# Optimization experiments

Hardware: AMD Instinct MI355X
Metric: run time of the kernel (lower is better)

Reference implementation:

```python
import jax, jax.numpy as jnp
import numpy as np

B, T, F, U = 64, 1024, 128, 256


def setup_inputs() -> dict:
    key = jax.random.key(0)
    k1, k2, k3 = jax.random.split(key, 3)
    inputs = jax.random.normal(k1, (B, T, F), dtype=jnp.float32)
    # R ~ Normal(stddev=1/time_horizon)
    R = jax.random.normal(k2, (F, U), dtype=jnp.float32) / T
    # W ~ Orthogonal init
    a = jax.random.normal(k3, (U, U), dtype=jnp.float32)
    q, r = jnp.linalg.qr(a)
    W = q * jnp.sign(jnp.diag(r))[None, :]
    bias = jnp.zeros((U,), dtype=jnp.float32)
    x0 = jnp.zeros((U,), dtype=jnp.float32)
    return {"inputs": inputs, "R": R, "W": W, "bias": bias, "x0": x0}


def reference(inputs, R, W, bias, x0):
    # inputs: [B, T, F]. Precompute input projections for all steps at once.
    h_all = jnp.einsum("btf,fu->tbu", inputs, R)  # [T, B, U]
    state0 = jnp.broadcast_to(x0, (inputs.shape[0], x0.shape[0]))  # [B, U]

    def step(state, h):
        new_state = jnp.tanh(h + state @ W + bias)
        return new_state, new_state

    _, states = jax.lax.scan(step, state0, h_all)  # states: [T, B, U]
    return states
```

## Files before the change

kernel.cpp:

```cpp
#include <hip/hip_runtime.h>
#include <hip/hip_bf16.h>

constexpr int B = 64;
constexpr int T = 1024;
constexpr int F = 128;
constexpr int U = 256;
constexpr int CH = 8;

__device__ __forceinline__ float toF32(float v) { return v; }
__device__ __forceinline__ float toF32(__hip_bfloat16 v) { return __bfloat162float(v); }

__device__ __forceinline__ void store8(float* p, const float* a) {
    ((float4*)p)[0] = make_float4(a[0], a[1], a[2], a[3]);
    ((float4*)p)[1] = make_float4(a[4], a[5], a[6], a[7]);
}
__device__ __forceinline__ void store8(__hip_bfloat16* p, const float* a) {
    unsigned int v[4];
    #pragma unroll
    for (int i = 0; i < 4; ++i) {
        __hip_bfloat16 lo = __float2bfloat16(a[2 * i]);
        __hip_bfloat16 hi = __float2bfloat16(a[2 * i + 1]);
        unsigned short lob = *(unsigned short*)&lo;
        unsigned short hib = *(unsigned short*)&hi;
        v[i] = (unsigned int)lob | ((unsigned int)hib << 16);
    }
    ((uint4*)p)[0] = make_uint4(v[0], v[1], v[2], v[3]);
}

__device__ __forceinline__ float rdlane(float v, int l) {
    return __uint_as_float(__builtin_amdgcn_readlane(__float_as_uint(v), l));
}

__device__ __forceinline__ float tanh_fast(float x) {
    float e = __builtin_amdgcn_exp2f(x * 2.885390081777927f);
    float r = __builtin_amdgcn_rcpf(1.0f + e);
    return fmaf(-2.0f, r, 1.0f);
}

__device__ __forceinline__ void lds_barrier() {
    __builtin_amdgcn_s_waitcnt(0xC07F);
    asm volatile("" ::: "memory");
    __builtin_amdgcn_s_barrier();
    asm volatile("" ::: "memory");
}

template <typename HT>
__global__ __launch_bounds__(512, 2) void proj_kernel(
    const float* __restrict__ in,
    const float* __restrict__ Rm,
    HT* __restrict__ h)
{
    const int t0   = blockIdx.x * 64;
    const int u0b  = blockIdx.y * 64;
    const int b    = blockIdx.z;
    const int tid  = threadIdx.x;
    const int lane = tid & 63;
    const int wv   = tid >> 6;
    const int u0   = __builtin_amdgcn_readfirstlane(u0b + wv * 8);

    __shared__ float4 a4[64 * 32];

    const float4* src = (const float4*)(in + ((size_t)b * T + t0) * F);
    #pragma unroll
    for (int it = 0; it < 4; ++it) {
        int f  = tid + it * 512;
        int r  = f >> 5;
        int k4 = f & 31;
        a4[(r << 5) | (k4 ^ (r & 31))] = src[f];
    }
    __syncthreads();

    const float* Rp = Rm + u0;
    float acc[8];
    #pragma unroll
    for (int j = 0; j < 8; ++j) acc[j] = 0.f;

    float ra[32], rb[32];
    #pragma unroll
    for (int kk = 0; kk < 4; ++kk)
        #pragma unroll
        for (int j = 0; j < 8; ++j)
            ra[kk * 8 + j] = Rp[(size_t)kk * U + j];

    const int r = lane;
    #pragma unroll
    for (int k4 = 0; k4 < 32; k4 += 2) {
        #pragma unroll
        for (int kk = 0; kk < 4; ++kk)
            #pragma unroll
            for (int j = 0; j < 8; ++j)
                rb[kk * 8 + j] = Rp[(size_t)((k4 + 1) * 4 + kk) * U + j];

        float4 av = a4[(r << 5) | (k4 ^ (r & 31))];
        #pragma unroll
        for (int j = 0; j < 8; ++j) {
            acc[j] = fmaf(av.x, ra[0 * 8 + j], acc[j]);
            acc[j] = fmaf(av.y, ra[1 * 8 + j], acc[j]);
            acc[j] = fmaf(av.z, ra[2 * 8 + j], acc[j]);
            acc[j] = fmaf(av.w, ra[3 * 8 + j], acc[j]);
        }

        if (k4 + 2 < 32) {
            #pragma unroll
            for (int kk = 0; kk < 4; ++kk)
                #pragma unroll
                for (int j = 0; j < 8; ++j)
                    ra[kk * 8 + j] = Rp[(size_t)((k4 + 2) * 4 + kk) * U + j];
        }

        float4 av2 = a4[(r << 5) | ((k4 + 1) ^ (r & 31))];
        #pragma unroll
        for (int j = 0; j < 8; ++j) {
            acc[j] = fmaf(av2.x, rb[0 * 8 + j], acc[j]);
            acc[j] = fmaf(av2.y, rb[1 * 8 + j], acc[j]);
            acc[j] = fmaf(av2.z, rb[2 * 8 + j], acc[j]);
            acc[j] = fmaf(av2.w, rb[3 * 8 + j], acc[j]);
        }
    }

    HT* hp = h + ((size_t)(t0 + r) * B + b) * U + u0;
    store8(hp, acc);
}

template <typename HT>
__global__ __launch_bounds__(512, 2) void rnn_kernel(
    const HT* __restrict__ h,
    const float* __restrict__ Wm,
    const float* __restrict__ bias,
    const float* __restrict__ x0,
    float* __restrict__ out)
{
    const int b    = blockIdx.x;
    const int tid  = threadIdx.x;
    const int l    = tid & 63;
    const int wv   = tid >> 6;
    const int k0   = wv << 5;

    __shared__ float p[2][8][256];

    float w0[32], w1[32], w2[32], w3[32];
    {
        const float* wp = Wm + (size_t)k0 * U + 4 * l;
        #pragma unroll
        for (int kk = 0; kk < 32; ++kk) {
            float4 v = *(const float4*)(wp + (size_t)kk * U);
            w0[kk] = v.x; w1[kk] = v.y; w2[kk] = v.z; w3[kk] = v.w;
        }
    }

    const bool act = (l < 32);
    const int  u   = k0 + (l & 31);
    const float bv = bias[u];

    float tv = x0[u];

    const size_t sT = (size_t)B * U;
    const HT* hp = h + (size_t)b * U + u;
    float* op = out + (size_t)b * U + u;

    float hc[CH], hn[CH], ob[CH];
    #pragma unroll
    for (int i = 0; i < CH; ++i) hc[i] = toF32(hp[(size_t)i * sT]);

    for (int tc = 0; tc < T; tc += CH) {
        if (tc + CH < T) {
            #pragma unroll
            for (int i = 0; i < CH; ++i)
                hn[i] = toF32(hp[(size_t)(tc + CH + i) * sT]);
        }
        if (tc > 0 && act) {
            #pragma unroll
            for (int i = 0; i < CH; ++i)
                op[(size_t)(tc - CH + i) * sT] = ob[i];
        }

        #pragma unroll
        for (int i = 0; i < CH; ++i) {
            float sb[32];
            #pragma unroll
            for (int kk = 0; kk < 32; ++kk) sb[kk] = rdlane(tv, kk);

            float a0 = 0.f, a1 = 0.f, a2 = 0.f, a3 = 0.f;
            #pragma unroll
            for (int kk = 0; kk < 32; ++kk) {
                a0 = fmaf(sb[kk], w0[kk], a0);
                a1 = fmaf(sb[kk], w1[kk], a1);
                a2 = fmaf(sb[kk], w2[kk], a2);
                a3 = fmaf(sb[kk], w3[kk], a3);
            }
            *(float4*)&p[i & 1][wv][4 * l] = make_float4(a0, a1, a2, a3);

            lds_barrier();

            float red = p[i & 1][0][u];
            #pragma unroll
            for (int w2i = 1; w2i < 8; ++w2i) red += p[i & 1][w2i][u];

            float val = tanh_fast(red + hc[i] + bv);
            ob[i] = val;
            tv = val;
        }

        if (tc + CH < T) {
            #pragma unroll
            for (int i = 0; i < CH; ++i) hc[i] = hn[i];
        }
    }

    if (act) {
        #pragma unroll
        for (int i = 0; i < CH; ++i)
            op[(size_t)(T - CH + i) * sT] = ob[i];
    }
}

extern "C" void kernel_launch(void* const* d_in, const int* in_sizes, int n_in,
                              void* d_out, int out_size, void* d_ws, size_t ws_size,
                              hipStream_t stream) {
    const float* in   = (const float*)d_in[0];
    const float* Rm   = (const float*)d_in[1];
    const float* Wm   = (const float*)d_in[2];
    const float* bias = (const float*)d_in[3];
    const float* x0   = (const float*)d_in[4];
    float* out = (float*)d_out;

    const size_t hElems = (size_t)T * B * U;
    dim3 pgrid(T / 64, U / 64, B);

    if (ws_size >= hElems * sizeof(float)) {
        float* h = (float*)d_ws;
        proj_kernel<float><<<pgrid, 512, 0, stream>>>(in, Rm, h);
        rnn_kernel<float><<<dim3(B), 512, 0, stream>>>(h, Wm, bias, x0, out);
    } else {
        __hip_bfloat16* h = (__hip_bfloat16*)d_ws;
        proj_kernel<__hip_bfloat16><<<pgrid, 512, 0, stream>>>(in, Rm, h);
        rnn_kernel<__hip_bfloat16><<<dim3(B), 512, 0, stream>>>(h, Wm, bias, x0, out);
    }
}
```

Baseline: 670.0 us.

## Use packed fp16 dot2 for recurrent matvec with DPP pair packing

Converts the W slice held in registers to packed fp16 pairs and computes the state-times-W product with v_dot2_f32_f16. The neighbouring lane's state comes in through a DPP swap, and each readlane broadcasts two fp16 values at once. This halves both readlanes and FMAs on the serial critical path and cuts weight register use. The change also folds the bias into the preloaded h values and reduces the cross-wave partials as a balanced tree. In exchange, state and weights are rounded to fp16 every step, which can accumulate error over the 1024-step recurrence.

```diff
diff --git a/kernel.cpp b/kernel.cpp
--- a/kernel.cpp
+++ b/kernel.cpp
@@ -6,6 +6,8 @@
 constexpr int F = 128;
 constexpr int U = 256;
 constexpr int CH = 8;
+
+typedef __fp16 h2 __attribute__((ext_vector_type(2)));
 
 __device__ __forceinline__ float toF32(float v) { return v; }
 __device__ __forceinline__ float toF32(__hip_bfloat16 v) { return __bfloat162float(v); }
@@ -27,8 +29,24 @@
     ((uint4*)p)[0] = make_uint4(v[0], v[1], v[2], v[3]);
 }
 
-__device__ __forceinline__ float rdlane(float v, int l) {
-    return __uint_as_float(__builtin_amdgcn_readlane(__float_as_uint(v), l));
+__device__ __forceinline__ unsigned int h2bits(h2 v) {
+    union { h2 h; unsigned int u; } c; c.h = v; return c.u;
+}
+__device__ __forceinline__ h2 bits2h(unsigned int u) {
+    union { unsigned int u; h2 h; } c; c.u = u; return c.h;
+}
+
+__device__ __forceinline__ h2 pk_rne(float a, float b) {
+    h2 v; v.x = (__fp16)a; v.y = (__fp16)b; return v;
+}
+
+__device__ __forceinline__ float fdot2(h2 a, h2 b, float c) {
+#if __has_builtin(__builtin_amdgcn_fdot2)
+    return __builtin_amdgcn_fdot2(a, b, c, false);
+#else
+    asm("v_dot2_f32_f16 %0, %1, %2, %0" : "+v"(c) : "v"(a), "v"(b));
+    return c;
+#endif
 }
 
 __device__ __forceinline__ float tanh_fast(float x) {
@@ -138,13 +156,17 @@
 
     __shared__ float p[2][8][256];
 
-    float w0[32], w1[32], w2[32], w3[32];
+    h2 wh[4][16];
     {
         const float* wp = Wm + (size_t)k0 * U + 4 * l;
         #pragma unroll
-        for (int kk = 0; kk < 32; ++kk) {
-            float4 v = *(const float4*)(wp + (size_t)kk * U);
-            w0[kk] = v.x; w1[kk] = v.y; w2[kk] = v.z; w3[kk] = v.w;
+        for (int m = 0; m < 16; ++m) {
+            float4 r0 = *(const float4*)(wp + (size_t)(2 * m) * U);
+            float4 r1 = *(const float4*)(wp + (size_t)(2 * m + 1) * U);
+            wh[0][m] = pk_rne(r0.x, r1.x);
+            wh[1][m] = pk_rne(r0.y, r1.y);
+            wh[2][m] = pk_rne(r0.z, r1.z);
+            wh[3][m] = pk_rne(r0.w, r1.w);
         }
     }
 
@@ -160,7 +182,7 @@
 
     float hc[CH], hn[CH], ob[CH];
     #pragma unroll
-    for (int i = 0; i < CH; ++i) hc[i] = toF32(hp[(size_t)i * sT]);
+    for (int i = 0; i < CH; ++i) hc[i] = toF32(hp[(size_t)i * sT]) + bv;
 
     for (int tc = 0; tc < T; tc += CH) {
         if (tc + CH < T) {
@@ -176,34 +198,39 @@
 
         #pragma unroll
         for (int i = 0; i < CH; ++i) {
-            float sb[32];
-            #pragma unroll
-            for (int kk = 0; kk < 32; ++kk) sb[kk] = rdlane(tv, kk);
+            float nb = __uint_as_float(__builtin_amdgcn_update_dpp(
+                0, (int)__float_as_uint(tv), 0xB1 ,
+                0xF, 0xF, true));
+            unsigned int pku = h2bits(pk_rne(tv, nb));
 
             float a0 = 0.f, a1 = 0.f, a2 = 0.f, a3 = 0.f;
             #pragma unroll
-            for (int kk = 0; kk < 32; ++kk) {
-                a0 = fmaf(sb[kk], w0[kk], a0);
-                a1 = fmaf(sb[kk], w1[kk], a1);
-                a2 = fmaf(sb[kk], w2[kk], a2);
-                a3 = fmaf(sb[kk], w3[kk], a3);
+            for (int m = 0; m < 16; ++m) {
+                h2 sh = bits2h(__builtin_amdgcn_readlane(pku, 2 * m));
+                a0 = fdot2(sh, wh[0][m], a0);
+                a1 = fdot2(sh, wh[1][m], a1);
+                a2 = fdot2(sh, wh[2][m], a2);
+                a3 = fdot2(sh, wh[3][m], a3);
             }
             *(float4*)&p[i & 1][wv][4 * l] = make_float4(a0, a1, a2, a3);
 
             lds_barrier();
 
-            float red = p[i & 1][0][u];
-            #pragma unroll
-            for (int w2i = 1; w2i < 8; ++w2i) red += p[i & 1][w2i][u];
-
-            float val = tanh_fast(red + hc[i] + bv);
+            const float* pb = &p[i & 1][0][u];
+            float q0 = pb[0 * 256], q1 = pb[1 * 256];
+            float q2 = pb[2 * 256], q3 = pb[3 * 256];
+            float q4 = pb[4 * 256], q5 = pb[5 * 256];
+            float q6 = pb[6 * 256], q7 = pb[7 * 256];
+            float red = ((q0 + q1) + (q2 + q3)) + ((q4 + q5) + (q6 + q7));
+
+            float val = tanh_fast(red + hc[i]);
             ob[i] = val;
             tv = val;
         }
 
         if (tc + CH < T) {
             #pragma unroll
-            for (int i = 0; i < CH; ++i) hc[i] = hn[i];
+            for (int i = 0; i < CH; ++i) hc[i] = hn[i] + bv;
         }
     }
 
```

After: 722.5 us. 1.08x slower.

## Batch 8 sequences per block and compute recurrence matmul with fp16 MFMA

Applied to the files above, without the earlier changes.

The recurrent kernel now processes 8 batch rows per workgroup and computes state@W with 16x16x32 fp16 MFMA instructions, with W held in registers as fp16 fragments. The state is exchanged through a swizzled double-buffered fp16 LDS tile with one barrier per step. This replaces the per-lane readlane broadcast, scalar FMAs and cross-wave LDS reduction, cutting per-step latency. The launch drops to 8 blocks, and using fp16 for the state and weights may introduce accuracy error across the long recurrence.

```diff
diff --git a/kernel.cpp b/kernel.cpp
--- a/kernel.cpp
+++ b/kernel.cpp
@@ -5,7 +5,9 @@
 constexpr int T = 1024;
 constexpr int F = 128;
 constexpr int U = 256;
-constexpr int CH = 8;
+
+typedef __fp16 f16x8 __attribute__((ext_vector_type(8)));
+typedef float  f32x4 __attribute__((ext_vector_type(4)));
 
 __device__ __forceinline__ float toF32(float v) { return v; }
 __device__ __forceinline__ float toF32(__hip_bfloat16 v) { return __bfloat162float(v); }
@@ -25,10 +27,6 @@
         v[i] = (unsigned int)lob | ((unsigned int)hib << 16);
     }
     ((uint4*)p)[0] = make_uint4(v[0], v[1], v[2], v[3]);
-}
-
-__device__ __forceinline__ float rdlane(float v, int l) {
-    return __uint_as_float(__builtin_amdgcn_readlane(__float_as_uint(v), l));
 }
 
 __device__ __forceinline__ float tanh_fast(float x) {
@@ -130,88 +128,105 @@
     const float* __restrict__ x0,
     float* __restrict__ out)
 {
-    const int b    = blockIdx.x;
-    const int tid  = threadIdx.x;
-    const int l    = tid & 63;
-    const int wv   = tid >> 6;
-    const int k0   = wv << 5;
-
-    __shared__ float p[2][8][256];
-
-    float w0[32], w1[32], w2[32], w3[32];
+    const int b0  = blockIdx.x * 8;
+    const int tid = threadIdx.x;
+    const int l   = tid & 63;
+    const int wv  = tid >> 6;
+    const int lr  = l & 15;
+    const int lg  = l >> 4;
+    const int n0  = wv * 32;
+
+    __shared__ __fp16 sbuf[2][16][256];
+
+    f16x8 bf0[8], bf1[8];
+    #pragma unroll
+    for (int kt = 0; kt < 8; ++kt) {
+        #pragma unroll
+        for (int jj = 0; jj < 8; ++jj) {
+            const size_t k = (size_t)(kt * 32 + lg * 8 + jj);
+            bf0[kt][jj] = (__fp16)Wm[k * U + n0 + lr];
+            bf1[kt][jj] = (__fp16)Wm[k * U + n0 + 16 + lr];
+        }
+    }
+
+    const bool  actv = (lg < 2);
+    const float bv0  = bias[n0 + lr];
+    const float bv1  = bias[n0 + 16 + lr];
+
     {
-        const float* wp = Wm + (size_t)k0 * U + 4 * l;
-        #pragma unroll
-        for (int kk = 0; kk < 32; ++kk) {
-            float4 v = *(const float4*)(wp + (size_t)kk * U);
-            w0[kk] = v.x; w1[kk] = v.y; w2[kk] = v.z; w3[kk] = v.w;
-        }
-    }
-
-    const bool act = (l < 32);
-    const int  u   = k0 + (l & 31);
-    const float bv = bias[u];
-
-    float tv = x0[u];
-
-    const size_t sT = (size_t)B * U;
-    const HT* hp = h + (size_t)b * U + u;
-    float* op = out + (size_t)b * U + u;
-
-    float hc[CH], hn[CH], ob[CH];
-    #pragma unroll
-    for (int i = 0; i < CH; ++i) hc[i] = toF32(hp[(size_t)i * sT]);
-
-    for (int tc = 0; tc < T; tc += CH) {
-        if (tc + CH < T) {
-            #pragma unroll
-            for (int i = 0; i < CH; ++i)
-                hn[i] = toF32(hp[(size_t)(tc + CH + i) * sT]);
-        }
-        if (tc > 0 && act) {
-            #pragma unroll
-            for (int i = 0; i < CH; ++i)
-                op[(size_t)(tc - CH + i) * sT] = ob[i];
-        }
-
-        #pragma unroll
-        for (int i = 0; i < CH; ++i) {
-            float sb[32];
-            #pragma unroll
-            for (int kk = 0; kk < 32; ++kk) sb[kk] = rdlane(tv, kk);
-
-            float a0 = 0.f, a1 = 0.f, a2 = 0.f, a3 = 0.f;
-            #pragma unroll
-            for (int kk = 0; kk < 32; ++kk) {
-                a0 = fmaf(sb[kk], w0[kk], a0);
-                a1 = fmaf(sb[kk], w1[kk], a1);
-                a2 = fmaf(sb[kk], w2[kk], a2);
-                a3 = fmaf(sb[kk], w3[kk], a3);
-            }
-            *(float4*)&p[i & 1][wv][4 * l] = make_float4(a0, a1, a2, a3);
-
-            lds_barrier();
-
-            float red = p[i & 1][0][u];
-            #pragma unroll
-            for (int w2i = 1; w2i < 8; ++w2i) red += p[i & 1][w2i][u];
-
-            float val = tanh_fast(red + hc[i] + bv);
-            ob[i] = val;
-            tv = val;
-        }
-
-        if (tc + CH < T) {
-            #pragma unroll
-            for (int i = 0; i < CH; ++i) hc[i] = hn[i];
-        }
-    }
-
-    if (act) {
-        #pragma unroll
-        for (int i = 0; i < CH; ++i)
-            op[(size_t)(T - CH + i) * sT] = ob[i];
-    }
+        const int m  = tid >> 5;
+        const int ub = (tid & 31) * 8;
+        #pragma unroll
+        for (int j = 0; j < 8; ++j)
+            sbuf[0][m][(ub + j) ^ ((m & 7) << 3)] = (__fp16)x0[ub + j];
+    }
+    __syncthreads();
+
+    const size_t tstride = (size_t)B * U;
+    const size_t base    = (size_t)(b0 + lg * 4) * U + lr;
+
+    HT hE[8], hO[8];
+    if (actv) {
+        #pragma unroll
+        for (int r = 0; r < 4; ++r) {
+            hE[r]     = h[base + (size_t)r * U + n0];
+            hE[4 + r] = h[base + (size_t)r * U + n0 + 16];
+            hO[r]     = h[tstride + base + (size_t)r * U + n0];
+            hO[4 + r] = h[tstride + base + (size_t)r * U + n0 + 16];
+        }
+    }
+
+#define RNN_STEP(t, hX, RB, WB)                                                   \
+    {                                                                             \
+        f32x4 acc0 = {0.f, 0.f, 0.f, 0.f}, acc1 = {0.f, 0.f, 0.f, 0.f};           \
+        if (actv) {                                                               \
+            _Pragma("unroll") for (int r = 0; r < 4; ++r) {                       \
+                acc0[r] = toF32(hX[r]) + bv0;                                     \
+                acc1[r] = toF32(hX[4 + r]) + bv1;                                 \
+            }                                                                     \
+            if ((t) + 2 < T) {                                                    \
+                const size_t o = (size_t)((t) + 2) * tstride + base;              \
+                _Pragma("unroll") for (int r = 0; r < 4; ++r) {                   \
+                    hX[r]     = h[o + (size_t)r * U + n0];                        \
+                    hX[4 + r] = h[o + (size_t)r * U + n0 + 16];                   \
+                }                                                                 \
+            }                                                                     \
+        }                                                                         \
+        f16x8 af[8];                                                              \
+        _Pragma("unroll") for (int kt = 0; kt < 8; ++kt)                          \
+            af[kt] = *(const f16x8*)&sbuf[RB][lr][(kt * 32 + lg * 8) ^            \
+                                                  ((lr & 7) << 3)];               \
+        _Pragma("unroll") for (int kt = 0; kt < 8; ++kt) {                        \
+            acc0 = __builtin_amdgcn_mfma_f32_16x16x32_f16(af[kt], bf0[kt],        \
+                                                          acc0, 0, 0, 0);         \
+            acc1 = __builtin_amdgcn_mfma_f32_16x16x32_f16(af[kt], bf1[kt],        \
+                                                          acc1, 0, 0, 0);         \
+        }                                                                         \
+        float v0[4], v1[4];                                                       \
+        _Pragma("unroll") for (int r = 0; r < 4; ++r) {                           \
+            v0[r] = tanh_fast(acc0[r]);                                           \
+            v1[r] = tanh_fast(acc1[r]);                                           \
+        }                                                                         \
+        if (actv) {                                                               \
+            const size_t o = (size_t)(t) * tstride + base;                        \
+            _Pragma("unroll") for (int r = 0; r < 4; ++r) {                       \
+                out[o + (size_t)r * U + n0]      = v0[r];                         \
+                out[o + (size_t)r * U + n0 + 16] = v1[r];                         \
+            }                                                                     \
+        }                                                                         \
+        _Pragma("unroll") for (int r = 0; r < 4; ++r) {                           \
+            const int m = lg * 4 + r;                                             \
+            sbuf[WB][m][(n0 + lr) ^ ((m & 7) << 3)]      = (__fp16)v0[r];         \
+            sbuf[WB][m][(n0 + 16 + lr) ^ ((m & 7) << 3)] = (__fp16)v1[r];         \
+        }                                                                         \
+        lds_barrier();                                                            \
+    }
+
+    for (int t = 0; t < T; t += 2) {
+        RNN_STEP(t,     hE, 0, 1)
+        RNN_STEP(t + 1, hO, 1, 0)
+    }
+#undef RNN_STEP
 }
 
 extern "C" void kernel_launch(void* const* d_in, const int* in_sizes, int n_in,
@@ -230,10 +245,10 @@
     if (ws_size >= hElems * sizeof(float)) {
         float* h = (float*)d_ws;
         proj_kernel<float><<<pgrid, 512, 0, stream>>>(in, Rm, h);
-        rnn_kernel<float><<<dim3(B), 512, 0, stream>>>(h, Wm, bias, x0, out);
+        rnn_kernel<float><<<dim3(8), 512, 0, stream>>>(h, Wm, bias, x0, out);
     } else {
         __hip_bfloat16* h = (__hip_bfloat16*)d_ws;
         proj_kernel<__hip_bfloat16><<<pgrid, 512, 0, stream>>>(in, Rm, h);
-        rnn_kernel<__hip_bfloat16><<<dim3(B), 512, 0, stream>>>(h, Wm, bias, x0, out);
-    }
-}
+        rnn_kernel<__hip_bfloat16><<<dim3(8), 512, 0, stream>>>(h, Wm, bias, x0, out);
+    }
+}
```

After: 1.150 ms. 1.72x slower.
